# Performance work log

Hardware: AMD Instinct MI355X
Metric: run time of the kernel (lower is better)

Reference implementation:

```python
import jax, jax.numpy as jnp
import numpy as np

B, P, D = 256, 128, 768        # batch, property slots per sample, encoder hidden dim
E = 64                          # num_properties (number of adapter heads)
H = 256                         # adapter_hidden_dim
H2 = H // 2
O = 2                           # output_dim
LN_EPS = 1e-5
RES_W_ADPT, RES_W_BASE = 0.7, 0.3


def setup_inputs() -> dict:
    key = jax.random.key(0)
    ks = jax.random.split(key, 12)
    hidden_states = jax.random.normal(ks[0], (B, P, D), dtype=jnp.float32)
    base_output = jax.random.normal(ks[1], (B, P, O), dtype=jnp.float32)
    properties = jax.random.randint(ks[2], (B, P), 0, E, dtype=jnp.int64)
    mask = (jax.random.uniform(ks[3], (B, P)) > 0.1).astype(jnp.float32)
    # Stacked per-head adapter parameters (LayerNorm + 3 Linears per head)
    ln_g = jnp.ones((E, D), dtype=jnp.float32)
    ln_b = jnp.zeros((E, D), dtype=jnp.float32)
    W1 = jax.random.normal(ks[4], (E, D, H), dtype=jnp.float32) * (1.0 / np.sqrt(D))
    b1 = jnp.zeros((E, H), dtype=jnp.float32)
    W2 = jax.random.normal(ks[5], (E, H, H2), dtype=jnp.float32) * (1.0 / np.sqrt(H))
    b2 = jnp.zeros((E, H2), dtype=jnp.float32)
    W3 = jax.random.normal(ks[6], (E, H2, O), dtype=jnp.float32) * 0.01  # init std=0.01 per source
    b3 = jnp.zeros((E, O), dtype=jnp.float32)
    return {
        "hidden_states": hidden_states, "base_output": base_output,
        "properties": properties, "mask": mask,
        "ln_g": ln_g, "ln_b": ln_b, "W1": W1, "b1": b1,
        "W2": W2, "b2": b2, "W3": W3, "b3": b3,
    }


def reference(hidden_states, base_output, properties, mask,
              ln_g, ln_b, W1, b1, W2, b2, W3, b3):
    b, p, d = hidden_states.shape
    o = W3.shape[-1]
    x = hidden_states.reshape(-1, d)                        # [N, D]
    # LayerNorm statistics are head-independent; only gamma/beta differ per head
    mu = jnp.mean(x, axis=-1, keepdims=True)
    var = jnp.mean((x - mu) ** 2, axis=-1, keepdims=True)
    xhat = (x - mu) * jax.lax.rsqrt(var + LN_EPS)           # [N, D]
    flat_p = properties.reshape(-1)                         # [N]
    flat_m = mask.reshape(-1)                               # [N]

    def body(acc, inp):
        idx, g, bt, w1, bb1, w2, bb2, w3, bb3 = inp
        h = jax.nn.relu((xhat * g + bt) @ w1 + bb1)         # [N, H]  (dropout = identity in eval)
        h = jax.nn.relu(h @ w2 + bb2)                       # [N, H2]
        out = h @ w3 + bb3                                  # [N, O]
        sel = (flat_p == idx) & (flat_m > 0)
        return jnp.where(sel[:, None], out, acc), None

    e = W1.shape[0]
    acc0 = jnp.zeros((b * p, o), dtype=x.dtype)
    acc, _ = jax.lax.scan(
        body, acc0,
        (jnp.arange(e), ln_g, ln_b, W1, b1, W2, b2, W3, b3))
    out = acc.reshape(b, p, o)
    out = RES_W_ADPT * out + RES_W_BASE * base_output       # use_residual=True
    return out * mask[..., None]
```

## Files before the change

kernel.cpp:

```cpp
#include <hip/hip_runtime.h>
#include <stdint.h>

typedef unsigned short u16;
typedef unsigned int   u32;

#define NTOK   32768
#define GD     768
#define GH     256
#define GH2    128
#define GE     64

typedef __bf16 bf16x8 __attribute__((ext_vector_type(8)));
typedef float  f32x4  __attribute__((ext_vector_type(4)));
union Frag { uint4 u; bf16x8 b; };

__device__ __forceinline__ float bf2f(u16 h) {
  union { u32 u; float f; } v; v.u = ((u32)h) << 16; return v.f;
}
__device__ __forceinline__ u16 f2bf(float f) {
  union { float f; u32 u; } v; v.f = f;
  u32 r = (v.u + 0x7fffu + ((v.u >> 16) & 1u)) >> 16;
  return (u16)r;
}

__device__ __forceinline__ void async16(void* lds, const void* g) {
  __builtin_amdgcn_global_load_lds(
      (const __attribute__((address_space(1))) void*)g,
      (__attribute__((address_space(3))) void*)lds, 16, 0, 0);
}

__device__ __forceinline__ int getProp(const int* p32, int t, int is64) {
  return is64 ? p32[2 * t] : p32[t];
}

static const size_t OFF_W1T  = 0;
static const size_t OFF_W2T  = 25165824;
static const size_t OFF_TOK  = 29360128;
static const size_t OFF_META = 29491200;

__global__ void setup_kernel(const int* __restrict__ prop, const float* __restrict__ mask,
                             u32* __restrict__ outz, int* __restrict__ counts2d,
                             int* __restrict__ cursors_p, int* __restrict__ flagp) {
  __shared__ int h[GE];
  __shared__ int vOr;
  const int b = blockIdx.x;
  const int tid = threadIdx.x;
  outz[b * 512 + tid] = 0u;
  outz[b * 512 + 256 + tid] = 0u;
  if (b < 4) cursors_p[b * 256 + tid] = 0;
  if (tid < GE) h[tid] = 0;
  if (tid == 0) vOr = 0;
  __syncthreads();
  int v = prop[2 * tid + 1] | prop[2 * (tid + 256) + 1];
  if (v) atomicOr(&vOr, 1);
  __syncthreads();
  const int is64 = (vOr == 0) ? 1 : 0;
  if (b == 0 && tid == 0) *flagp = is64;
  const int t = b * 256 + tid;
  if (mask[t] > 0.f) atomicAdd(&h[getProp(prop, t, is64)], 1);
  __syncthreads();
  if (tid < GE) counts2d[b * GE + tid] = h[tid];
}

__global__ void transpose_w1(const float* __restrict__ in, u16* __restrict__ out) {
  __shared__ u16 tl[64][260];
  const int bid = blockIdx.x;
  const int e  = bid / 12, r = bid % 12;
  const int d0 = (r / 4) * 256, h0 = (r % 4) * 64;
  const int tid = threadIdx.x;
  const size_t inMat = (size_t)e * GD * GH;
  const size_t outMat = (size_t)e * GH * GD;
  const int h_l = (tid & 15) * 4, d_l = tid >> 4;
#pragma unroll
  for (int dd = 0; dd < 16; ++dd) {
    const int d = d_l + dd * 16;
    float4 v = *(const float4*)(in + inMat + (size_t)(d0 + d) * GH + h0 + h_l);
    tl[h_l + 0][d] = f2bf(v.x);
    tl[h_l + 1][d] = f2bf(v.y);
    tl[h_l + 2][d] = f2bf(v.z);
    tl[h_l + 3][d] = f2bf(v.w);
  }
  __syncthreads();
  const int wv = tid >> 6, ln = tid & 63;
  const int d_glob = d0 + ln * 4;
  const size_t tbase = outMat + (size_t)(d_glob >> 5) * 8192 +
                       (size_t)((d_glob >> 3) & 3) * 2048 + (d_glob & 7);
#pragma unroll
  for (int hh = 0; hh < 16; ++hh) {
    const int h = wv * 16 + hh;
    *(uint2*)(out + tbase + (size_t)(h0 + h) * 8) = *(const uint2*)&tl[h][ln * 4];
  }
}

__global__ void transpose_w2(const float* __restrict__ in, u16* __restrict__ out) {
  __shared__ u16 tile[32][33];
  const int tilesPerMat = 32;
  const int e  = blockIdx.x / tilesPerMat;
  const int t  = blockIdx.x % tilesPerMat;
  const int tr = t / 4, tc = t % 4;
  const size_t mat = (size_t)e * GH * GH2;
  const int tx = threadIdx.x & 31, ty = threadIdx.x >> 5;
  const int r0 = tr * 32, c0 = tc * 32;
#pragma unroll
  for (int i = 0; i < 32; i += 8)
    tile[ty + i][tx] = f2bf(in[mat + (size_t)(r0 + ty + i) * GH2 + c0 + tx]);
  __syncthreads();
  const int k = r0 + tx;
  const size_t kbase = mat + (size_t)(k >> 5) * 4096 +
                       (size_t)((k >> 3) & 3) * 1024 + (k & 7);
#pragma unroll
  for (int i = 0; i < 32; i += 8)
    out[kbase + (size_t)(c0 + ty + i) * 8] = tile[tx][ty + i];
}

__global__ void scan_kernel(const int* __restrict__ counts2d, int* __restrict__ offsets,
                            int* __restrict__ tileHead, int* __restrict__ tileRow,
                            int* __restrict__ nTilesPtr) {
  __shared__ int part[4][GE];
  const int tid = threadIdx.x;
  const int e = tid & 63, q = tid >> 6;
  int c = 0;
  for (int b = q * 32; b < q * 32 + 32; ++b) c += counts2d[b * GE + e];
  part[q][e] = c;
  __syncthreads();
  if (tid < GE) {
    const int ct = part[0][e] + part[1][e] + part[2][e] + part[3][e];
    int inc = ct;
#pragma unroll
    for (int d = 1; d < 64; d <<= 1) { int n = __shfl_up(inc, d); if (e >= d) inc += n; }
    const int off = inc - ct;
    offsets[e] = off;
    if (e == 63) offsets[64] = inc;
    int ntile = (ct + 63) >> 6;
    int inct = ntile;
#pragma unroll
    for (int d = 1; d < 64; d <<= 1) { int n = __shfl_up(inct, d); if (e >= d) inct += n; }
    const int tb = inct - ntile;
    for (int j = 0; j < ntile; ++j) { tileHead[tb + j] = e; tileRow[tb + j] = off + j * 64; }
    if (e == 63) *nTilesPtr = inct;
  }
}

__global__ void scatter_kernel(const int* __restrict__ prop, const float* __restrict__ mask,
                               const int* __restrict__ offsets, int* __restrict__ cursors_p,
                               int* __restrict__ tokenIds, const int* __restrict__ flag) {
  __shared__ int h[GE];
  __shared__ int basebin[GE];
  const int tid = threadIdx.x;
  const int t = blockIdx.x * 256 + tid;
  if (tid < GE) h[tid] = 0;
  __syncthreads();
  int p = -1, rank = 0;
  if (mask[t] > 0.f) {
    p = getProp(prop, t, *flag);
    rank = atomicAdd(&h[p], 1);
  }
  __syncthreads();
  if (tid < GE && h[tid] > 0) basebin[tid] = atomicAdd(&cursors_p[tid * 16], h[tid]);
  __syncthreads();
  if (p >= 0) tokenIds[offsets[p] + basebin[p] + rank] = t;
}

__global__ __launch_bounds__(256, 2) void adapter_gemm(
    const float* __restrict__ hs, const u16* __restrict__ w1t, const u16* __restrict__ w2t,
    const float* __restrict__ lng, const float* __restrict__ lnb,
    const float* __restrict__ b1, const float* __restrict__ b2,
    const float* __restrict__ w3, const float* __restrict__ b3,
    const float* __restrict__ base, const float* __restrict__ mask,
    const int* __restrict__ tokenIds, const int* __restrict__ offsets,
    const int* __restrict__ tileHead, const int* __restrict__ tileRow,
    const int* __restrict__ nTilesPtr, float* __restrict__ outp) {
  __shared__ union LU {
    struct { u16 A[2][2048]; u16 B[2][8192]; } s;
    u16 h[17408];
  } uni;
  __shared__ u16 sB2[2][4096];
  __shared__ float sBias1[256];
  __shared__ float sBias2[128];
  __shared__ float sW3[2][128];
  __shared__ float sB3[2];
  __shared__ int   sTok[64];
  __shared__ __align__(16) float sGam[GD];
  __shared__ __align__(16) float sBet[GD];
  __shared__ float sMu[64];
  __shared__ float sRstd[64];

  const int tid  = threadIdx.x;
  const int wv   = tid >> 6;
  const int ln   = tid & 63;
  const int l15  = tid & 15;
  const int quad = (tid & 63) >> 4;
  const f32x4 vzero = {0.f, 0.f, 0.f, 0.f};
  const int nt = *nTilesPtr;
  const int qq = nt >> 3, rr = nt & 7;

  for (int i = blockIdx.x; i < nt; i += gridDim.x) {
    const int x = i & 7, s = i >> 3;
    const int tile = (x < rr ? x * (qq + 1) : rr * (qq + 1) + (x - rr) * qq) + s;

    __syncthreads();
    const int e  = tileHead[tile];
    const int rs = tileRow[tile];
    const int nRows = min(64, offsets[e + 1] - rs);

    if (tid < 64) sTok[tid] = tokenIds[rs + min(tid, nRows - 1)];
    sBias1[tid] = b1[e * GH + tid];
    if (tid < 128) sBias2[tid] = b2[e * GH2 + tid];
    { const int k = tid >> 1, o = tid & 1; sW3[o][k] = w3[e * GH2 * 2 + k * 2 + o]; }
    if (tid < 2) sB3[tid] = b3[e * 2 + tid];
    __syncthreads();

    const u16* w1e = w1t + (size_t)e * GH * GD;
    const u16* w2e = w2t + (size_t)e * GH2 * GH;

#pragma unroll
    for (int j = 0; j < 4; ++j)
      async16(uni.s.B[0] + wv * 2048 + j * 512,
              w1e + wv * 2048 + j * 512 + ln * 8);

    if (tid < 192) {
      *(float4*)&sGam[tid * 4] = *(const float4*)(lng + (size_t)e * GD + tid * 4);
      *(float4*)&sBet[tid * 4] = *(const float4*)(lnb + (size_t)e * GD + tid * 4);
    }

#pragma unroll 2
    for (int pass = 0; pass < 4; ++pass) {
      const int row = pass * 16 + (tid >> 4);
      const int l16 = tid & 15;
      const float* xp = hs + (size_t)sTok[row] * GD + l16 * 4;
      float sm = 0.f, sq = 0.f;
#pragma unroll
      for (int c = 0; c < 12; ++c) {
        float4 u = *(const float4*)(xp + c * 64);
        sm += u.x + u.y + u.z + u.w;
        sq += u.x*u.x + u.y*u.y + u.z*u.z + u.w*u.w;
      }
#pragma unroll
      for (int d = 1; d < 16; d <<= 1) { sm += __shfl_xor(sm, d); sq += __shfl_xor(sq, d); }
      if (l16 == 0) {
        const float mu = sm * (1.f / 768.f);
        sMu[row] = mu;
        sRstd[row] = rsqrtf(sq * (1.f / 768.f) - mu * mu + 1e-5f);
      }
    }
    __syncthreads();

    const int r0  = tid >> 3;
    const int klo = (tid & 7) * 4;
    const int kgrp = klo >> 3, kin = klo & 7;
    const float* xA = hs + (size_t)sTok[r0] * GD + klo;
    const float* xB = hs + (size_t)sTok[r0 + 32] * GD + klo;
    const float muA = sMu[r0],      rsA = sRstd[r0];
    const float muB = sMu[r0 + 32], rsB = sRstd[r0 + 32];

#define STAGE_A(K0, PAR) do {                                                   \
    const float4 gv = *(const float4*)&sGam[(K0) + klo];                        \
    const float4 bv = *(const float4*)&sBet[(K0) + klo];                        \
    float4 va = *(const float4*)(xA + (K0));                                    \
    float4 vb = *(const float4*)(xB + (K0));                                    \
    uint2 oa, ob;                                                               \
    oa.x = (u32)f2bf((va.x - muA) * rsA * gv.x + bv.x)                          \
         | ((u32)f2bf((va.y - muA) * rsA * gv.y + bv.y) << 16);                 \
    oa.y = (u32)f2bf((va.z - muA) * rsA * gv.z + bv.z)                          \
         | ((u32)f2bf((va.w - muA) * rsA * gv.w + bv.w) << 16);                 \
    ob.x = (u32)f2bf((vb.x - muB) * rsB * gv.x + bv.x)                          \
         | ((u32)f2bf((vb.y - muB) * rsB * gv.y + bv.y) << 16);                 \
    ob.y = (u32)f2bf((vb.z - muB) * rsB * gv.z + bv.z)                          \
         | ((u32)f2bf((vb.w - muB) * rsB * gv.w + bv.w) << 16);                 \
    *(uint2*)&uni.s.A[PAR][kgrp * 512 + r0 * 8 + kin] = oa;                     \
    *(uint2*)&uni.s.A[PAR][kgrp * 512 + (r0 + 32) * 8 + kin] = ob;              \
  } while (0)

    f32x4 acc1[4][4];
#pragma unroll
    for (int f = 0; f < 4; ++f)
#pragma unroll
      for (int g = 0; g < 4; ++g) acc1[f][g] = vzero;

    STAGE_A(0, 0);

    for (int kt = 0; kt < 24; ++kt) {
      __syncthreads();
      if (kt + 1 < 24) {
        const int par = (kt + 1) & 1;
#pragma unroll
        for (int j = 0; j < 4; ++j)
          async16(uni.s.B[par] + wv * 2048 + j * 512,
                  w1e + (kt + 1) * 8192 + wv * 2048 + j * 512 + ln * 8);
        STAGE_A((kt + 1) * 32, par);
      }
      const int par = kt & 1;
      Frag fa[4], fb[4];
#pragma unroll
      for (int f = 0; f < 4; ++f)
        fa[f].u = *(const uint4*)&uni.s.A[par][quad * 512 + (f * 16 + l15) * 8];
#pragma unroll
      for (int g = 0; g < 4; ++g)
        fb[g].u = *(const uint4*)&uni.s.B[par][quad * 2048 + (wv * 64 + g * 16 + l15) * 8];
#pragma unroll
      for (int f = 0; f < 4; ++f)
#pragma unroll
        for (int g = 0; g < 4; ++g)
          acc1[f][g] = __builtin_amdgcn_mfma_f32_16x16x32_bf16(fa[f].b, fb[g].b, acc1[f][g], 0, 0, 0);
    }
    __syncthreads();

#pragma unroll
    for (int j = 0; j < 2; ++j)
      async16(sB2[0] + wv * 1024 + j * 512,
              w2e + wv * 1024 + j * 512 + ln * 8);

#pragma unroll
    for (int f = 0; f < 4; ++f)
#pragma unroll
      for (int g = 0; g < 4; ++g) {
        const int col = wv * 64 + g * 16 + l15;
        const float bias = sBias1[col];
#pragma unroll
        for (int r = 0; r < 4; ++r) {
          const int row = f * 16 + quad * 4 + r;
          uni.h[row * 264 + col] = f2bf(fmaxf(acc1[f][g][r] + bias, 0.f));
        }
      }

    f32x4 acc2[4][2];
#pragma unroll
    for (int f = 0; f < 4; ++f)
#pragma unroll
      for (int g = 0; g < 2; ++g) acc2[f][g] = vzero;

    for (int kt = 0; kt < 8; ++kt) {
      __syncthreads();
      if (kt + 1 < 8) {
        const int par = (kt + 1) & 1;
#pragma unroll
        for (int j = 0; j < 2; ++j)
          async16(sB2[par] + wv * 1024 + j * 512,
                  w2e + (kt + 1) * 4096 + wv * 1024 + j * 512 + ln * 8);
      }
      const int par = kt & 1;
      Frag fa2[4], fb2[2];
#pragma unroll
      for (int f = 0; f < 4; ++f)
        fa2[f].u = *(const uint4*)&uni.h[(f * 16 + l15) * 264 + kt * 32 + quad * 8];
#pragma unroll
      for (int g = 0; g < 2; ++g)
        fb2[g].u = *(const uint4*)&sB2[par][quad * 1024 + (wv * 32 + g * 16 + l15) * 8];
#pragma unroll
      for (int f = 0; f < 4; ++f)
#pragma unroll
        for (int g = 0; g < 2; ++g)
          acc2[f][g] = __builtin_amdgcn_mfma_f32_16x16x32_bf16(fa2[f].b, fb2[g].b, acc2[f][g], 0, 0, 0);
    }
    __syncthreads();

#pragma unroll
    for (int f = 0; f < 4; ++f)
#pragma unroll
      for (int g = 0; g < 2; ++g) {
        const int col = wv * 32 + g * 16 + l15;
        const float bias = sBias2[col];
#pragma unroll
        for (int r = 0; r < 4; ++r) {
          const int row = f * 16 + quad * 4 + r;
          uni.h[row * 130 + col] = f2bf(fmaxf(acc2[f][g][r] + bias, 0.f));
        }
      }
    __syncthreads();

    const int m = tid >> 1, o = tid & 1;
    if (m < nRows) {
      float a = sB3[o];
      const u16* h2row = &uni.h[m * 130];
#pragma unroll 16
      for (int k = 0; k < 128; ++k) a += bf2f(h2row[k]) * sW3[o][k];
      const int t = sTok[m];
      const float mk = mask[t];
      const float bs = base[t * 2 + o];
      outp[t * 2 + o] = (0.7f * a + 0.3f * bs) * mk;
    }
  }
#undef STAGE_A
}

extern "C" void kernel_launch(void* const* d_in, const int* in_sizes, int n_in,
                              void* d_out, int out_size, void* d_ws, size_t ws_size,
                              hipStream_t stream) {
  const float* hs   = (const float*)d_in[0];
  const float* base = (const float*)d_in[1];
  const int*   prop = (const int*)d_in[2];
  const float* mask = (const float*)d_in[3];
  const float* lng  = (const float*)d_in[4];
  const float* lnb  = (const float*)d_in[5];
  const float* W1   = (const float*)d_in[6];
  const float* b1   = (const float*)d_in[7];
  const float* W2   = (const float*)d_in[8];
  const float* b2   = (const float*)d_in[9];
  const float* W3   = (const float*)d_in[10];
  const float* b3   = (const float*)d_in[11];

  char* ws = (char*)d_ws;
  u16* w1t  = (u16*)(ws + OFF_W1T);
  u16* w2t  = (u16*)(ws + OFF_W2T);
  int* tok  = (int*)(ws + OFF_TOK);
  int* meta = (int*)(ws + OFF_META);
  int* counts2d  = meta;
  int* offsets   = meta + 8192;
  int* tileHead  = meta + 8320;
  int* tileRow   = meta + 9344;
  int* nTiles    = meta + 10368;
  int* propFlag  = meta + 10369;
  int* cursors_p = meta + 10432;

  setup_kernel<<<128, 256, 0, stream>>>(prop, mask, (u32*)d_out, counts2d,
                                        cursors_p, propFlag);
  transpose_w1<<<768, 256, 0, stream>>>(W1, w1t);
  transpose_w2<<<64 * 32, 256, 0, stream>>>(W2, w2t);
  scan_kernel<<<1, 256, 0, stream>>>(counts2d, offsets, tileHead, tileRow, nTiles);
  scatter_kernel<<<NTOK / 256, 256, 0, stream>>>(prop, mask, offsets, cursors_p, tok, propFlag);
  adapter_gemm<<<640, 256, 0, stream>>>(hs, w1t, w2t, lng, lnb, b1, b2, W3, b3,
                                        base, mask, tok, offsets, tileHead, tileRow,
                                        nTiles, (float*)d_out);
}
```

Before: 260.7 us.

## Triple-buffer GEMM1 pipeline with register prefetch and direct W2 register loads

Converts the first GEMM's double-buffered LDS pipeline into a three-stage ring, issuing W1 async copies and activation global loads two iterations ahead and holding the prefetched activations in registers. Synchronisation becomes explicit vmcnt/lgkmcnt waits plus raw s_barrier with sched barriers, so each barrier waits only on what it needs. W2 fragments are loaded straight from global memory into registers (16 fragments per thread) instead of being staged through a separate LDS buffer, which frees that shared memory. The aim is to hide global load latency behind MFMA work. In exchange it raises register pressure under launch_bounds(256,2) and relies on hand-counted vmcnt values being correct.

```diff
diff --git a/kernel.cpp b/kernel.cpp
--- a/kernel.cpp
+++ b/kernel.cpp
@@ -27,6 +27,13 @@
   __builtin_amdgcn_global_load_lds(
       (const __attribute__((address_space(1))) void*)g,
       (__attribute__((address_space(3))) void*)lds, 16, 0, 0);
+}
+
+__device__ __forceinline__ void bar_lds() {
+  asm volatile("s_waitcnt lgkmcnt(0)" ::: "memory");
+  __builtin_amdgcn_sched_barrier(0);
+  __builtin_amdgcn_s_barrier();
+  __builtin_amdgcn_sched_barrier(0);
 }
 
 __device__ __forceinline__ int getProp(const int* p32, int t, int is64) {
@@ -171,10 +178,9 @@
     const int* __restrict__ tileHead, const int* __restrict__ tileRow,
     const int* __restrict__ nTilesPtr, float* __restrict__ outp) {
   __shared__ union LU {
-    struct { u16 A[2][2048]; u16 B[2][8192]; } s;
+    struct { u16 A[3][2048]; u16 B[3][8192]; } s;
     u16 h[17408];
   } uni;
-  __shared__ u16 sB2[2][4096];
   __shared__ float sBias1[256];
   __shared__ float sBias2[128];
   __shared__ float sW3[2][128];
@@ -213,15 +219,33 @@
     const u16* w1e = w1t + (size_t)e * GH * GD;
     const u16* w2e = w2t + (size_t)e * GH2 * GH;
 
-#pragma unroll
-    for (int j = 0; j < 4; ++j)
-      async16(uni.s.B[0] + wv * 2048 + j * 512,
-              w1e + wv * 2048 + j * 512 + ln * 8);
-
     if (tid < 192) {
       *(float4*)&sGam[tid * 4] = *(const float4*)(lng + (size_t)e * GD + tid * 4);
       *(float4*)&sBet[tid * 4] = *(const float4*)(lnb + (size_t)e * GD + tid * 4);
     }
+
+    const int r0  = tid >> 3;
+    const int klo = (tid & 7) * 4;
+    const int kgrp = klo >> 3, kin = klo & 7;
+    const float* xA = hs + (size_t)sTok[r0] * GD + klo;
+    const float* xB = hs + (size_t)sTok[r0 + 32] * GD + klo;
+
+#define ISSUE_B(S, KT) do {                                                     \
+    u16* _bb = uni.s.B[S] + wv * 2048;                                          \
+    const u16* _gg = w1e + (KT) * 8192 + wv * 2048 + ln * 8;                    \
+    async16(_bb,        _gg);        async16(_bb + 512,  _gg + 512);            \
+    async16(_bb + 1024, _gg + 1024); async16(_bb + 1536, _gg + 1536);           \
+  } while (0)
+
+    float4 pAa[2], pAb[2];
+    ISSUE_B(0, 0);
+    __builtin_amdgcn_sched_barrier(0);
+    pAa[0] = *(const float4*)(xA);
+    pAb[0] = *(const float4*)(xB);
+    ISSUE_B(1, 1);
+    __builtin_amdgcn_sched_barrier(0);
+    pAa[1] = *(const float4*)(xA + 32);
+    pAb[1] = *(const float4*)(xB + 32);
 
 #pragma unroll 2
     for (int pass = 0; pass < 4; ++pass) {
@@ -243,53 +267,39 @@
         sRstd[row] = rsqrtf(sq * (1.f / 768.f) - mu * mu + 1e-5f);
       }
     }
-    __syncthreads();
-
-    const int r0  = tid >> 3;
-    const int klo = (tid & 7) * 4;
-    const int kgrp = klo >> 3, kin = klo & 7;
-    const float* xA = hs + (size_t)sTok[r0] * GD + klo;
-    const float* xB = hs + (size_t)sTok[r0 + 32] * GD + klo;
+    bar_lds();
+
     const float muA = sMu[r0],      rsA = sRstd[r0];
     const float muB = sMu[r0 + 32], rsB = sRstd[r0 + 32];
 
-#define STAGE_A(K0, PAR) do {                                                   \
+#define XFORM_WRITE(PAR, AA, BB, K0) do {                                       \
     const float4 gv = *(const float4*)&sGam[(K0) + klo];                        \
     const float4 bv = *(const float4*)&sBet[(K0) + klo];                        \
-    float4 va = *(const float4*)(xA + (K0));                                    \
-    float4 vb = *(const float4*)(xB + (K0));                                    \
     uint2 oa, ob;                                                               \
-    oa.x = (u32)f2bf((va.x - muA) * rsA * gv.x + bv.x)                          \
-         | ((u32)f2bf((va.y - muA) * rsA * gv.y + bv.y) << 16);                 \
-    oa.y = (u32)f2bf((va.z - muA) * rsA * gv.z + bv.z)                          \
-         | ((u32)f2bf((va.w - muA) * rsA * gv.w + bv.w) << 16);                 \
-    ob.x = (u32)f2bf((vb.x - muB) * rsB * gv.x + bv.x)                          \
-         | ((u32)f2bf((vb.y - muB) * rsB * gv.y + bv.y) << 16);                 \
-    ob.y = (u32)f2bf((vb.z - muB) * rsB * gv.z + bv.z)                          \
-         | ((u32)f2bf((vb.w - muB) * rsB * gv.w + bv.w) << 16);                 \
+    oa.x = (u32)f2bf((AA.x - muA) * rsA * gv.x + bv.x)                          \
+         | ((u32)f2bf((AA.y - muA) * rsA * gv.y + bv.y) << 16);                 \
+    oa.y = (u32)f2bf((AA.z - muA) * rsA * gv.z + bv.z)                          \
+         | ((u32)f2bf((AA.w - muA) * rsA * gv.w + bv.w) << 16);                 \
+    ob.x = (u32)f2bf((BB.x - muB) * rsB * gv.x + bv.x)                          \
+         | ((u32)f2bf((BB.y - muB) * rsB * gv.y + bv.y) << 16);                 \
+    ob.y = (u32)f2bf((BB.z - muB) * rsB * gv.z + bv.z)                          \
+         | ((u32)f2bf((BB.w - muB) * rsB * gv.w + bv.w) << 16);                 \
     *(uint2*)&uni.s.A[PAR][kgrp * 512 + r0 * 8 + kin] = oa;                     \
     *(uint2*)&uni.s.A[PAR][kgrp * 512 + (r0 + 32) * 8 + kin] = ob;              \
   } while (0)
 
+    XFORM_WRITE(0, pAa[0], pAb[0], 0);
+    bar_lds();
+
     f32x4 acc1[4][4];
 #pragma unroll
     for (int f = 0; f < 4; ++f)
 #pragma unroll
       for (int g = 0; g < 4; ++g) acc1[f][g] = vzero;
 
-    STAGE_A(0, 0);
-
+#pragma unroll
     for (int kt = 0; kt < 24; ++kt) {
-      __syncthreads();
-      if (kt + 1 < 24) {
-        const int par = (kt + 1) & 1;
-#pragma unroll
-        for (int j = 0; j < 4; ++j)
-          async16(uni.s.B[par] + wv * 2048 + j * 512,
-                  w1e + (kt + 1) * 8192 + wv * 2048 + j * 512 + ln * 8);
-        STAGE_A((kt + 1) * 32, par);
-      }
-      const int par = kt & 1;
+      const int par = kt % 3;
       Frag fa[4], fb[4];
 #pragma unroll
       for (int f = 0; f < 4; ++f)
@@ -297,18 +307,36 @@
 #pragma unroll
       for (int g = 0; g < 4; ++g)
         fb[g].u = *(const uint4*)&uni.s.B[par][quad * 2048 + (wv * 64 + g * 16 + l15) * 8];
+      if (kt + 2 < 24) {
+        ISSUE_B((kt + 2) % 3, kt + 2);
+        __builtin_amdgcn_sched_barrier(0);
+        pAa[kt & 1] = *(const float4*)(xA + (kt + 2) * 32);
+        pAb[kt & 1] = *(const float4*)(xB + (kt + 2) * 32);
+      }
 #pragma unroll
       for (int f = 0; f < 4; ++f)
 #pragma unroll
         for (int g = 0; g < 4; ++g)
           acc1[f][g] = __builtin_amdgcn_mfma_f32_16x16x32_bf16(fa[f].b, fb[g].b, acc1[f][g], 0, 0, 0);
+      if (kt + 1 < 24)
+        XFORM_WRITE((kt + 1) % 3, pAa[(kt + 1) & 1], pAb[(kt + 1) & 1], (kt + 1) * 32);
+      if (kt < 22) {
+        asm volatile("s_waitcnt vmcnt(6)" ::: "memory");
+      } else {
+        asm volatile("s_waitcnt vmcnt(0)" ::: "memory");
+      }
+      __builtin_amdgcn_sched_barrier(0);
+      bar_lds();
     }
-    __syncthreads();
-
-#pragma unroll
-    for (int j = 0; j < 2; ++j)
-      async16(sB2[0] + wv * 1024 + j * 512,
-              w2e + wv * 1024 + j * 512 + ln * 8);
+    bar_lds();
+
+    Frag bW2[8][2];
+#pragma unroll
+    for (int kt = 0; kt < 8; ++kt)
+#pragma unroll
+      for (int g = 0; g < 2; ++g)
+        bW2[kt][g].u = *(const uint4*)(w2e + kt * 4096 + quad * 1024 +
+                                       (size_t)(wv * 32 + g * 16 + l15) * 8);
 
 #pragma unroll
     for (int f = 0; f < 4; ++f)
@@ -322,6 +350,7 @@
           uni.h[row * 264 + col] = f2bf(fmaxf(acc1[f][g][r] + bias, 0.f));
         }
       }
+    bar_lds();
 
     f32x4 acc2[4][2];
 #pragma unroll
@@ -329,30 +358,19 @@
 #pragma unroll
       for (int g = 0; g < 2; ++g) acc2[f][g] = vzero;
 
+#pragma unroll
     for (int kt = 0; kt < 8; ++kt) {
-      __syncthreads();
-      if (kt + 1 < 8) {
-        const int par = (kt + 1) & 1;
-#pragma unroll
-        for (int j = 0; j < 2; ++j)
-          async16(sB2[par] + wv * 1024 + j * 512,
-                  w2e + (kt + 1) * 4096 + wv * 1024 + j * 512 + ln * 8);
-      }
-      const int par = kt & 1;
-      Frag fa2[4], fb2[2];
+      Frag fa2[4];
 #pragma unroll
       for (int f = 0; f < 4; ++f)
         fa2[f].u = *(const uint4*)&uni.h[(f * 16 + l15) * 264 + kt * 32 + quad * 8];
 #pragma unroll
-      for (int g = 0; g < 2; ++g)
-        fb2[g].u = *(const uint4*)&sB2[par][quad * 1024 + (wv * 32 + g * 16 + l15) * 8];
-#pragma unroll
       for (int f = 0; f < 4; ++f)
 #pragma unroll
         for (int g = 0; g < 2; ++g)
-          acc2[f][g] = __builtin_amdgcn_mfma_f32_16x16x32_bf16(fa2[f].b, fb2[g].b, acc2[f][g], 0, 0, 0);
+          acc2[f][g] = __builtin_amdgcn_mfma_f32_16x16x32_bf16(fa2[f].b, bW2[kt][g].b, acc2[f][g], 0, 0, 0);
     }
-    __syncthreads();
+    bar_lds();
 
 #pragma unroll
     for (int f = 0; f < 4; ++f)
@@ -366,7 +384,7 @@
           uni.h[row * 130 + col] = f2bf(fmaxf(acc2[f][g][r] + bias, 0.f));
         }
       }
-    __syncthreads();
+    bar_lds();
 
     const int m = tid >> 1, o = tid & 1;
     if (m < nRows) {
@@ -380,7 +398,8 @@
       outp[t * 2 + o] = (0.7f * a + 0.3f * bs) * mk;
     }
   }
-#undef STAGE_A
+#undef XFORM_WRITE
+#undef ISSUE_B
 }
 
 extern "C" void kernel_launch(void* const* d_in, const int* in_sizes, int n_in,
```

Measured after the change: 255.1 us. 1.02x faster.
